# Kernel optimization log

Hardware: AMD Instinct MI355X
Metric: run time of the kernel (lower is better)

## Reference

```python
import jax, jax.numpy as jnp
import numpy as np

T, B, I, H = 512, 64, 1024, 1024


def setup_inputs() -> dict:
    key = jax.random.key(0)
    ks = jax.random.split(key, 9)
    k = 1.0 / np.sqrt(H)  # PyTorch LSTMCell init scale
    u = lambda kk, shape: jax.random.uniform(kk, shape, jnp.float32, -k, k)
    return dict(
        input_=jax.random.normal(ks[0], (T, B, I), jnp.float32),
        w_ih0=u(ks[1], (4 * H, I)),
        w_hh0=u(ks[2], (4 * H, H)),
        b_ih0=u(ks[3], (4 * H,)),
        b_hh0=u(ks[4], (4 * H,)),
        w_ih1=u(ks[5], (4 * H, H)),
        w_hh1=u(ks[6], (4 * H, H)),
        b_ih1=u(ks[7], (4 * H,)),
        b_hh1=u(ks[8], (4 * H,)),
    )


def _lstm_layer(x, w_ih, w_hh, b):
    """x: [T,B,in] -> outputs h over time [T,B,H]. Gate order i,f,g,o (PyTorch)."""
    h_dim = w_hh.shape[1]
    # Precompute input contribution for all timesteps in one big GEMM.
    xw = jnp.einsum('tbi,gi->tbg', x, w_ih) + b  # [T,B,4H]

    def step(carry, xw_t):
        h, c = carry
        gates = xw_t + h @ w_hh.T  # [B,4H]
        i, f, g, o = jnp.split(gates, 4, axis=-1)
        c_next = jax.nn.sigmoid(f) * c + jax.nn.sigmoid(i) * jnp.tanh(g)
        h_next = jax.nn.sigmoid(o) * jnp.tanh(c_next)
        return (h_next, c_next), h_next

    h0 = jnp.zeros((x.shape[1], h_dim), x.dtype)
    _, out = jax.lax.scan(step, (h0, h0), xw)
    return out


def reference(input_, w_ih0, w_hh0, b_ih0, b_hh0, w_ih1, w_hh1, b_ih1, b_hh1):
    # eval mode: GumbelNoise (p=0), dropout, and wdrop are identities
    h1 = _lstm_layer(input_, w_ih0, w_hh0, b_ih0 + b_hh0)
    h2 = _lstm_layer(h1, w_ih1, w_hh1, b_ih1 + b_hh1)
    return h2  # [T,B,H]
```

## Files before the change

kernel.cpp:

```cpp
#include <hip/hip_runtime.h>


typedef _Float16 h8_t __attribute__((ext_vector_type(8)));
typedef _Float16 h4_t __attribute__((ext_vector_type(4)));
typedef float f4_t __attribute__((ext_vector_type(4)));

#define T_STEPS 512
#define BATCH 64
#define HID 1024
#define STEP_ELEMS (BATCH * HID)


__global__ void k_f32_to_f16(const float* __restrict__ src, _Float16* __restrict__ dst) {
    size_t i = ((size_t)blockIdx.x * blockDim.x + threadIdx.x) * 4;
    float4 v = *(const float4*)(src + i);
    h4_t h = { (_Float16)v.x, (_Float16)v.y, (_Float16)v.z, (_Float16)v.w };
    *(h4_t*)(dst + i) = h;
}

__global__ void k_build_wcat(const float* __restrict__ w_ih, const float* __restrict__ w_hh,
                             _Float16* __restrict__ wcat) {
    size_t i = ((size_t)blockIdx.x * blockDim.x + threadIdx.x) * 4;
    int n = (int)(i >> 11);
    int k = (int)(i & 2047);
    const float* src = (k < 1024) ? (w_ih + (size_t)n * 1024 + k)
                                  : (w_hh + (size_t)n * 1024 + (k - 1024));
    float4 v = *(const float4*)src;
    h4_t h = { (_Float16)v.x, (_Float16)v.y, (_Float16)v.z, (_Float16)v.w };
    *(h4_t*)(wcat + i) = h;
}

__global__ void k_bias(const float* __restrict__ a, const float* __restrict__ b,
                       float* __restrict__ o) {
    int i = blockIdx.x * blockDim.x + threadIdx.x;
    o[i] = a[i] + b[i];
}

__device__ __forceinline__ float sigmf(float x) { return 1.0f / (1.0f + __expf(-x)); }
__device__ __forceinline__ float tanh_fast(float x) {
    x = fminf(fmaxf(x, -15.f), 15.f);
    float e = __expf(2.f * x);
    return (e - 1.f) / (e + 1.f);
}


__device__ __forceinline__ void wait_flags(const unsigned* __restrict__ flags,
                                           unsigned target) {
    const int tid = threadIdx.x;
    for (;;) {
        unsigned v = target;
        if (tid < 128)
            v = __hip_atomic_load(&flags[tid], __ATOMIC_RELAXED,
                                  __HIP_MEMORY_SCOPE_AGENT);
        if (__syncthreads_and((int)(v >= target))) break;
        __builtin_amdgcn_s_sleep(1);
    }
}

__device__ __forceinline__ void publish_flag(unsigned* __restrict__ flag, unsigned val) {
    asm volatile("s_waitcnt vmcnt(0)" ::: "memory");
    __syncthreads();
    if (threadIdx.x == 0)
        __hip_atomic_store(flag, val, __ATOMIC_RELAXED, __HIP_MEMORY_SCOPE_AGENT);
}


__device__ __forceinline__ void do_phase(f4_t& a0e, f4_t& a0o, f4_t& a1e, f4_t& a1o,
                                         const _Float16* __restrict__ src, int aoff,
                                         const char* __restrict__ lb, int lds_base) {
    h8_t buf[2][4];
#pragma unroll
    for (int j = 0; j < 4; ++j)
        buf[0][j] = *(const h8_t*)(src + aoff + j * 32);
#pragma unroll
    for (int c = 0; c < 8; ++c) {
        if (c < 7) {
#pragma unroll
            for (int j = 0; j < 4; ++j)
                buf[(c + 1) & 1][j] = *(const h8_t*)(src + aoff + (c * 4 + 4 + j) * 32);
        }
#pragma unroll
        for (int j = 0; j < 4; ++j) {
            const int kk = c * 4 + j;
            h8_t b0 = *(const h8_t*)(lb + lds_base + kk * 2048);
            h8_t b1 = *(const h8_t*)(lb + lds_base + kk * 2048 + 256);
            if (kk & 1) {
                a0o = __builtin_amdgcn_mfma_f32_16x16x32_f16(buf[c & 1][j], b0, a0o, 0, 0, 0);
                a1o = __builtin_amdgcn_mfma_f32_16x16x32_f16(buf[c & 1][j], b1, a1o, 0, 0, 0);
            } else {
                a0e = __builtin_amdgcn_mfma_f32_16x16x32_f16(buf[c & 1][j], b0, a0e, 0, 0, 0);
                a1e = __builtin_amdgcn_mfma_f32_16x16x32_f16(buf[c & 1][j], b1, a1e, 0, 0, 0);
            }
        }
    }
}

__global__ __launch_bounds__(256, 1) void lstm_persist(
    const _Float16* __restrict__ x16, _Float16* __restrict__ h1,
    _Float16* __restrict__ h2, float* __restrict__ out,
    const _Float16* __restrict__ wc0, const _Float16* __restrict__ wc1,
    const float* __restrict__ bias0, const float* __restrict__ bias1,
    unsigned* __restrict__ f0, unsigned* __restrict__ f1)
{
    extern __shared__ char smem[];
    const int blk = blockIdx.x;
    const int layer = blk >> 7;
    const int u0 = (blk & 127) * 8;
    const _Float16* __restrict__ wc = layer ? wc1 : wc0;
    const float* __restrict__ bias = layer ? bias1 : bias0;
    const int tid = threadIdx.x;

    {
        const int kk = tid >> 2, qq = tid & 3;
#pragma unroll 4
        for (int C = 0; C < 32; ++C) {
            const int n = ((C >> 3) << 10) + u0 + (C & 7);
            h8_t v = *(const h8_t*)(wc + (size_t)n * 2048 + (size_t)kk * 32 + qq * 8);
            const int p = qq ^ (C & 3);
            *(h8_t*)(smem + kk * 2048 + p * 512 + C * 16) = v;
        }
    }
    __syncthreads();

    const int lane = tid & 63;
    const int wave = tid >> 6;
    const int q = lane >> 4;
    const int m16 = lane & 15;
    const int unit = u0 + (m16 & 7);
    const bool lo8 = (m16 & 8) == 0;

    const float bi = bias[unit];
    const float bf = bias[1024 + unit];
    const float bg = bias[2048 + unit];
    const float bo = bias[3072 + unit];

    const char* __restrict__ lb = smem + ((q ^ (m16 & 3)) * 512 + m16 * 16);
    const int aoff = (wave * 16 + m16) * 1024 + q * 8;

    float cst[4] = {0.f, 0.f, 0.f, 0.f};

    if (layer == 0) {
        unsigned* myflag = &f0[blk];
        for (int s = 0; s < T_STEPS; ++s) {
            f4_t a0e = {0.f,0.f,0.f,0.f}, a0o = {0.f,0.f,0.f,0.f};
            f4_t a1e = {0.f,0.f,0.f,0.f}, a1o = {0.f,0.f,0.f,0.f};
            do_phase(a0e, a0o, a1e, a1o, x16 + (size_t)s * STEP_ELEMS, aoff, lb, 0);
            if (s) {
                wait_flags(f0, (unsigned)s);
                do_phase(a0e, a0o, a1e, a1o,
                         h1 + (size_t)(s - 1) * STEP_ELEMS, aoff, lb, 65536);
            }
            const f4_t acc0 = a0e + a0o;
            const f4_t acc1 = a1e + a1o;
            _Float16* __restrict__ hout = h1 + (size_t)s * STEP_ELEMS;
#pragma unroll
            for (int ri = 0; ri < 4; ++ri) {
                const float p0 = __shfl_xor(acc0[ri], 8, 64);
                const float p1 = __shfl_xor(acc1[ri], 8, 64);
                const float iv = (lo8 ? acc0[ri] : p0) + bi;
                const float fv = (lo8 ? p0 : acc0[ri]) + bf;
                const float gv = (lo8 ? acc1[ri] : p1) + bg;
                const float ov = (lo8 ? p1 : acc1[ri]) + bo;
                const float cn = sigmf(fv) * cst[ri] + sigmf(iv) * tanh_fast(gv);
                const float hn = sigmf(ov) * tanh_fast(cn);
                cst[ri] = cn;
                if (lo8) {
                    const size_t idx = (size_t)((wave * 16 + q * 4 + ri) * HID + unit);
                    const unsigned short hb =
                        __builtin_bit_cast(unsigned short, (_Float16)hn);
                    __hip_atomic_store((unsigned short*)(hout + idx), hb,
                                       __ATOMIC_RELAXED, __HIP_MEMORY_SCOPE_AGENT);
                }
            }
            publish_flag(myflag, (unsigned)(s + 1));
        }
    } else {
        unsigned* myflag = &f1[blk & 127];
        for (int t = 0; t < T_STEPS; ++t) {
            wait_flags(f0, (unsigned)(t + 1));
            if (t) wait_flags(f1, (unsigned)t);
            f4_t a0e = {0.f,0.f,0.f,0.f}, a0o = {0.f,0.f,0.f,0.f};
            f4_t a1e = {0.f,0.f,0.f,0.f}, a1o = {0.f,0.f,0.f,0.f};
            do_phase(a0e, a0o, a1e, a1o, h1 + (size_t)t * STEP_ELEMS, aoff, lb, 0);
            if (t)
                do_phase(a0e, a0o, a1e, a1o,
                         h2 + (size_t)(t - 1) * STEP_ELEMS, aoff, lb, 65536);
            const f4_t acc0 = a0e + a0o;
            const f4_t acc1 = a1e + a1o;
            _Float16* __restrict__ hout = h2 + (size_t)t * STEP_ELEMS;
            float* __restrict__ oout = out + (size_t)t * STEP_ELEMS;
#pragma unroll
            for (int ri = 0; ri < 4; ++ri) {
                const float p0 = __shfl_xor(acc0[ri], 8, 64);
                const float p1 = __shfl_xor(acc1[ri], 8, 64);
                const float iv = (lo8 ? acc0[ri] : p0) + bi;
                const float fv = (lo8 ? p0 : acc0[ri]) + bf;
                const float gv = (lo8 ? acc1[ri] : p1) + bg;
                const float ov = (lo8 ? p1 : acc1[ri]) + bo;
                const float cn = sigmf(fv) * cst[ri] + sigmf(iv) * tanh_fast(gv);
                const float hn = sigmf(ov) * tanh_fast(cn);
                cst[ri] = cn;
                if (lo8) {
                    const size_t idx = (size_t)((wave * 16 + q * 4 + ri) * HID + unit);
                    const unsigned short hb =
                        __builtin_bit_cast(unsigned short, (_Float16)hn);
                    __hip_atomic_store((unsigned short*)(hout + idx), hb,
                                       __ATOMIC_RELAXED, __HIP_MEMORY_SCOPE_AGENT);
                    oout[idx] = hn;
                }
            }
            publish_flag(myflag, (unsigned)(t + 1));
        }
    }
}


__global__ __launch_bounds__(256) void lstm_step2(
    const _Float16* __restrict__ xin0, const _Float16* __restrict__ hp0,
    const _Float16* __restrict__ wc0, const float* __restrict__ bb0,
    float* __restrict__ cb0, _Float16* __restrict__ ho0,
    const _Float16* __restrict__ xin1, const _Float16* __restrict__ hp1,
    const _Float16* __restrict__ wc1, const float* __restrict__ bb1,
    float* __restrict__ cb1, _Float16* __restrict__ ho1,
    float* __restrict__ of1, int mask)
{
    int blk = blockIdx.x;
    const _Float16 *xin, *hp, *wc;
    const float* bb;
    float* cbuf;
    _Float16* hf;
    float* hf32 = nullptr;
    int u0;
    if (blk < 64) {
        if (!(mask & 1)) return;
        xin = xin0; hp = hp0; wc = wc0; bb = bb0; cbuf = cb0; hf = ho0;
        u0 = blk * 16;
    } else {
        if (!(mask & 2)) return;
        xin = xin1; hp = hp1; wc = wc1; bb = bb1; cbuf = cb1; hf = ho1;
        hf32 = of1;
        u0 = (blk - 64) * 16;
    }

    const int lane = threadIdx.x & 63;
    const int wave = threadIdx.x >> 6;
    const int q = lane >> 4;
    const int m16 = lane & 15;
    const int r = wave * 16 + m16;

    f4_t acc[4] = {};
    const _Float16* wrow[4];
#pragma unroll
    for (int g = 0; g < 4; ++g)
        wrow[g] = wc + (size_t)(g * 1024 + u0 + m16) * 2048 + q * 8;

    {
        const _Float16* arow = xin + (size_t)r * 1024 + q * 8;
#pragma unroll 4
        for (int kk = 0; kk < 32; ++kk) {
            h8_t a = *(const h8_t*)(arow + kk * 32);
#pragma unroll
            for (int g = 0; g < 4; ++g) {
                h8_t b = *(const h8_t*)(wrow[g] + kk * 32);
                acc[g] = __builtin_amdgcn_mfma_f32_16x16x32_f16(a, b, acc[g], 0, 0, 0);
            }
        }
    }
    {
        const _Float16* arow = hp + (size_t)r * 1024 + q * 8;
#pragma unroll 4
        for (int kk = 0; kk < 32; ++kk) {
            h8_t a = *(const h8_t*)(arow + kk * 32);
#pragma unroll
            for (int g = 0; g < 4; ++g) {
                h8_t b = *(const h8_t*)(wrow[g] + 1024 + kk * 32);
                acc[g] = __builtin_amdgcn_mfma_f32_16x16x32_f16(a, b, acc[g], 0, 0, 0);
            }
        }
    }

    const int unit = u0 + m16;
    const float bi = bb[unit];
    const float bf = bb[1024 + unit];
    const float bg = bb[2048 + unit];
    const float bo = bb[3072 + unit];
#pragma unroll
    for (int ri = 0; ri < 4; ++ri) {
        int row = wave * 16 + q * 4 + ri;
        float iv = acc[0][ri] + bi;
        float fv = acc[1][ri] + bf;
        float gv = acc[2][ri] + bg;
        float ov = acc[3][ri] + bo;
        size_t idx = (size_t)row * HID + unit;
        float cn = sigmf(fv) * cbuf[idx] + sigmf(iv) * tanhf(gv);
        float hn = sigmf(ov) * tanhf(cn);
        cbuf[idx] = cn;
        hf[idx] = (_Float16)hn;
        if (hf32) hf32[idx] = hn;
    }
}


extern "C" void kernel_launch(void* const* d_in, const int* in_sizes, int n_in,
                              void* d_out, int out_size, void* d_ws, size_t ws_size,
                              hipStream_t stream) {
    const float* input = (const float*)d_in[0];
    const float* w_ih0 = (const float*)d_in[1];
    const float* w_hh0 = (const float*)d_in[2];
    const float* b_ih0 = (const float*)d_in[3];
    const float* b_hh0 = (const float*)d_in[4];
    const float* w_ih1 = (const float*)d_in[5];
    const float* w_hh1 = (const float*)d_in[6];
    const float* b_ih1 = (const float*)d_in[7];
    const float* b_hh1 = (const float*)d_in[8];
    float* outp = (float*)d_out;

    char* p = (char*)d_ws;
    _Float16* x16 = (_Float16*)p;  p += (size_t)T_STEPS * STEP_ELEMS * 2;
    _Float16* h1  = (_Float16*)p;  p += (size_t)T_STEPS * STEP_ELEMS * 2;
    _Float16* h2  = (_Float16*)p;  p += (size_t)T_STEPS * STEP_ELEMS * 2;
    _Float16* wc0 = (_Float16*)p;  p += (size_t)4096 * 2048 * 2;
    _Float16* wc1 = (_Float16*)p;  p += (size_t)4096 * 2048 * 2;
    float* bias0  = (float*)p;     p += 4096 * 4;
    float* bias1  = (float*)p;     p += 4096 * 4;
    float* c0     = (float*)p;     p += STEP_ELEMS * 4;
    float* c1     = (float*)p;     p += STEP_ELEMS * 4;
    _Float16* hz  = (_Float16*)p;  p += STEP_ELEMS * 2;
    unsigned* f0  = (unsigned*)p;  p += 512;
    unsigned* f1  = (unsigned*)p;  p += 512;

    hipMemsetAsync(c0, 0, STEP_ELEMS * 4, stream);
    hipMemsetAsync(c1, 0, STEP_ELEMS * 4, stream);
    hipMemsetAsync(hz, 0, STEP_ELEMS * 2, stream);
    hipMemsetAsync(f0, 0, 1024, stream);

    k_f32_to_f16<<<(T_STEPS * STEP_ELEMS / 4) / 256, 256, 0, stream>>>(input, x16);
    k_build_wcat<<<(4096 * 2048 / 4) / 256, 256, 0, stream>>>(w_ih0, w_hh0, wc0);
    k_build_wcat<<<(4096 * 2048 / 4) / 256, 256, 0, stream>>>(w_ih1, w_hh1, wc1);
    k_bias<<<16, 256, 0, stream>>>(b_ih0, b_hh0, bias0);
    k_bias<<<16, 256, 0, stream>>>(b_ih1, b_hh1, bias1);

    void* params[] = { (void*)&x16, (void*)&h1, (void*)&h2, (void*)&outp,
                       (void*)&wc0, (void*)&wc1, (void*)&bias0, (void*)&bias1,
                       (void*)&f0, (void*)&f1 };
    hipError_t ce = hipLaunchCooperativeKernel((const void*)lstm_persist,
                                               dim3(256), dim3(256),
                                               params, 131072u, stream);
    if (ce != hipSuccess) {
        for (int s = 0; s <= T_STEPS; ++s) {
            int t1 = (s > 0) ? (s - 1) : 0;
            const _Float16* xin0 = x16 + (size_t)s * STEP_ELEMS;
            const _Float16* hp0  = (s == 0) ? hz : h1 + (size_t)(s - 1) * STEP_ELEMS;
            _Float16* ho0        = h1 + (size_t)s * STEP_ELEMS;
            const _Float16* xin1 = h1 + (size_t)t1 * STEP_ELEMS;
            const _Float16* hp1  = (t1 == 0) ? hz : h2 + (size_t)(t1 - 1) * STEP_ELEMS;
            _Float16* ho1        = h2 + (size_t)t1 * STEP_ELEMS;
            float* of1           = outp + (size_t)t1 * STEP_ELEMS;
            int mask = ((s < T_STEPS) ? 1 : 0) | ((s >= 1) ? 2 : 0);
            if (s == T_STEPS) xin0 = x16;
            lstm_step2<<<128, 256, 0, stream>>>(xin0, hp0, wc0, bias0, c0, ho0,
                                                xin1, hp1, wc1, bias1, c1, ho1,
                                                of1, mask);
        }
    }
}
```

Measured before the change: 7.146 ms.

## Issue all 32 A-fragment loads up front and split layer-1 flag waits

Replaces the double-buffered chunked load/MFMA loop with one pass that issues all 32 global loads of the A operand into registers before running the 32 MFMA pairs. The aim is to put every load in flight at once and cut the per-step latency of the recurrent chain. Layer 1 now waits only on the layer-0 flag before its input phase and waits on its own flag just before the recurrent phase, so the h1 contribution overlaps with waiting on peer blocks. Holding 32 h8 registers raises register pressure, but one wave per SIMD is already assumed.

```diff
diff --git a/kernel.cpp b/kernel.cpp
--- a/kernel.cpp
+++ b/kernel.cpp
@@ -65,35 +65,30 @@
 }
 
 
-__device__ __forceinline__ void do_phase(f4_t& a0e, f4_t& a0o, f4_t& a1e, f4_t& a1o,
-                                         const _Float16* __restrict__ src, int aoff,
-                                         const char* __restrict__ lb, int lds_base) {
-    h8_t buf[2][4];
-#pragma unroll
-    for (int j = 0; j < 4; ++j)
-        buf[0][j] = *(const h8_t*)(src + aoff + j * 32);
-#pragma unroll
-    for (int c = 0; c < 8; ++c) {
-        if (c < 7) {
-#pragma unroll
-            for (int j = 0; j < 4; ++j)
-                buf[(c + 1) & 1][j] = *(const h8_t*)(src + aoff + (c * 4 + 4 + j) * 32);
-        }
-#pragma unroll
-        for (int j = 0; j < 4; ++j) {
-            const int kk = c * 4 + j;
-            h8_t b0 = *(const h8_t*)(lb + lds_base + kk * 2048);
-            h8_t b1 = *(const h8_t*)(lb + lds_base + kk * 2048 + 256);
-            if (kk & 1) {
-                a0o = __builtin_amdgcn_mfma_f32_16x16x32_f16(buf[c & 1][j], b0, a0o, 0, 0, 0);
-                a1o = __builtin_amdgcn_mfma_f32_16x16x32_f16(buf[c & 1][j], b1, a1o, 0, 0, 0);
-            } else {
-                a0e = __builtin_amdgcn_mfma_f32_16x16x32_f16(buf[c & 1][j], b0, a0e, 0, 0, 0);
-                a1e = __builtin_amdgcn_mfma_f32_16x16x32_f16(buf[c & 1][j], b1, a1e, 0, 0, 0);
-            }
-        }
-    }
-}
+__device__ __forceinline__ void issue32(h8_t* __restrict__ areg,
+                                        const _Float16* __restrict__ src, int aoff) {
+#pragma unroll
+    for (int kk = 0; kk < 32; ++kk)
+        areg[kk] = *(const h8_t*)(src + aoff + kk * 32);
+}
+
+__device__ __forceinline__ void mfma32(f4_t& a0e, f4_t& a0o, f4_t& a1e, f4_t& a1o,
+                                       const h8_t* __restrict__ areg,
+                                       const char* __restrict__ lb, int lds_base) {
+#pragma unroll
+    for (int kk = 0; kk < 32; ++kk) {
+        h8_t b0 = *(const h8_t*)(lb + lds_base + kk * 2048);
+        h8_t b1 = *(const h8_t*)(lb + lds_base + kk * 2048 + 256);
+        if (kk & 1) {
+            a0o = __builtin_amdgcn_mfma_f32_16x16x32_f16(areg[kk], b0, a0o, 0, 0, 0);
+            a1o = __builtin_amdgcn_mfma_f32_16x16x32_f16(areg[kk], b1, a1o, 0, 0, 0);
+        } else {
+            a0e = __builtin_amdgcn_mfma_f32_16x16x32_f16(areg[kk], b0, a0e, 0, 0, 0);
+            a1e = __builtin_amdgcn_mfma_f32_16x16x32_f16(areg[kk], b1, a1e, 0, 0, 0);
+        }
+    }
+}
+
 
 __global__ __launch_bounds__(256, 1) void lstm_persist(
     const _Float16* __restrict__ x16, _Float16* __restrict__ h1,
@@ -142,13 +137,15 @@
     if (layer == 0) {
         unsigned* myflag = &f0[blk];
         for (int s = 0; s < T_STEPS; ++s) {
+            h8_t areg[32];
             f4_t a0e = {0.f,0.f,0.f,0.f}, a0o = {0.f,0.f,0.f,0.f};
             f4_t a1e = {0.f,0.f,0.f,0.f}, a1o = {0.f,0.f,0.f,0.f};
-            do_phase(a0e, a0o, a1e, a1o, x16 + (size_t)s * STEP_ELEMS, aoff, lb, 0);
+            issue32(areg, x16 + (size_t)s * STEP_ELEMS, aoff);
+            mfma32(a0e, a0o, a1e, a1o, areg, lb, 0);
             if (s) {
                 wait_flags(f0, (unsigned)s);
-                do_phase(a0e, a0o, a1e, a1o,
-                         h1 + (size_t)(s - 1) * STEP_ELEMS, aoff, lb, 65536);
+                issue32(areg, h1 + (size_t)(s - 1) * STEP_ELEMS, aoff);
+                mfma32(a0e, a0o, a1e, a1o, areg, lb, 65536);
             }
             const f4_t acc0 = a0e + a0o;
             const f4_t acc1 = a1e + a1o;
@@ -177,14 +174,17 @@
     } else {
         unsigned* myflag = &f1[blk & 127];
         for (int t = 0; t < T_STEPS; ++t) {
-            wait_flags(f0, (unsigned)(t + 1));
-            if (t) wait_flags(f1, (unsigned)t);
+            h8_t areg[32];
             f4_t a0e = {0.f,0.f,0.f,0.f}, a0o = {0.f,0.f,0.f,0.f};
             f4_t a1e = {0.f,0.f,0.f,0.f}, a1o = {0.f,0.f,0.f,0.f};
-            do_phase(a0e, a0o, a1e, a1o, h1 + (size_t)t * STEP_ELEMS, aoff, lb, 0);
-            if (t)
-                do_phase(a0e, a0o, a1e, a1o,
-                         h2 + (size_t)(t - 1) * STEP_ELEMS, aoff, lb, 65536);
+            wait_flags(f0, (unsigned)(t + 1));
+            issue32(areg, h1 + (size_t)t * STEP_ELEMS, aoff);
+            mfma32(a0e, a0o, a1e, a1o, areg, lb, 0);
+            if (t) {
+                wait_flags(f1, (unsigned)t);
+                issue32(areg, h2 + (size_t)(t - 1) * STEP_ELEMS, aoff);
+                mfma32(a0e, a0o, a1e, a1o, areg, lb, 65536);
+            }
             const f4_t acc0 = a0e + a0o;
             const f4_t acc1 = a1e + a1o;
             _Float16* __restrict__ hout = h2 + (size_t)t * STEP_ELEMS;
```

New measurement: 7.140 ms. About the same (-0.1%).
